# Kernel optimization log

Measured on AMD Instinct MI355X. Metric: run time of the kernel, lower is better.

## Reference

```python
import math
import jax, jax.numpy as jnp
import numpy as np

B, T, IDIM, D, H, L, DFF, CHUNK, LEFT = 8, 1024, 80, 512, 8, 6, 2048, 16, 4
DK = D // H
EPS = 1e-12  # espnet LayerNorm eps


def setup_inputs() -> dict:
    key = jax.random.key(0)
    it = iter(jax.random.split(key, 40))
    def nrm(shape, s=0.02):
        return jax.random.normal(next(it), shape, jnp.float32) * s
    return {
        "xs": jax.random.normal(next(it), (B, T, IDIM), jnp.float32),
        "masks": jnp.ones((B, 1, T), jnp.bool_),
        "emb_w": nrm((IDIM, D)), "emb_b": jnp.zeros((D,), jnp.float32),
        "emb_g": jnp.ones((D,), jnp.float32), "emb_beta": jnp.zeros((D,), jnp.float32),
        "wq": nrm((L, D, D)), "bq": jnp.zeros((L, D), jnp.float32),
        "wk": nrm((L, D, D)), "bk": jnp.zeros((L, D), jnp.float32),
        "wv": nrm((L, D, D)), "bv": jnp.zeros((L, D), jnp.float32),
        "wo": nrm((L, D, D)), "bo": jnp.zeros((L, D), jnp.float32),
        "ln1_g": jnp.ones((L, D), jnp.float32), "ln1_b": jnp.zeros((L, D), jnp.float32),
        "ln2_g": jnp.ones((L, D), jnp.float32), "ln2_b": jnp.zeros((L, D), jnp.float32),
        "ff1_w": nrm((L, D, DFF)), "ff1_b": jnp.zeros((L, DFF), jnp.float32),
        "ff2_w": nrm((L, DFF, D)), "ff2_b": jnp.zeros((L, D), jnp.float32),
        "fin_g": jnp.ones((D,), jnp.float32), "fin_b": jnp.zeros((D,), jnp.float32),
    }


def _ln(x, g, b):
    m = jnp.mean(x, -1, keepdims=True)
    v = jnp.mean((x - m) ** 2, -1, keepdims=True)
    return (x - m) / jnp.sqrt(v + EPS) * g + b


def _posenc(x):
    t, d = x.shape[1], x.shape[2]
    pos = jnp.arange(t, dtype=jnp.float32)[:, None]
    div = jnp.exp(jnp.arange(0, d, 2, dtype=jnp.float32) * (-math.log(10000.0) / d))
    pe = jnp.zeros((t, d), x.dtype)
    pe = pe.at[:, 0::2].set(jnp.sin(pos * div)).at[:, 1::2].set(jnp.cos(pos * div))
    return x * math.sqrt(d) + pe


def _mha(x, mask, wq, bq, wk, bk, wv, bv, wo, bo):
    b, t, _ = x.shape
    def split(w, bias):
        return (x @ w + bias).reshape(b, t, H, DK).transpose(0, 2, 1, 3)
    q, k, v = split(wq, bq), split(wk, bk), split(wv, bv)
    scores = jnp.einsum('bhqd,bhkd->bhqk', q, k) / math.sqrt(DK)
    m = mask[:, None]  # (B,1,1,T) for padding mask, (B,1,T,T) for chunk mask
    scores = jnp.where(m, scores, jnp.finfo(scores.dtype).min)
    attn = jnp.where(m, jax.nn.softmax(scores, axis=-1), 0.0)
    out = jnp.einsum('bhqk,bhkd->bhqd', attn, v).transpose(0, 2, 1, 3).reshape(b, t, D)
    return out @ wo + bo


def _stack(x, mask, p):
    # pre-norm (normalize_before=True, concat_after=False), dropout=0 (eval)
    for i in range(L):
        r = x
        h = _ln(x, p['ln1_g'][i], p['ln1_b'][i])
        x = r + _mha(h, mask, p['wq'][i], p['bq'][i], p['wk'][i], p['bk'][i],
                     p['wv'][i], p['bv'][i], p['wo'][i], p['bo'][i])
        r = x
        h = _ln(x, p['ln2_g'][i], p['ln2_b'][i])
        x = r + (jax.nn.relu(h @ p['ff1_w'][i] + p['ff1_b'][i]) @ p['ff2_w'][i] + p['ff2_b'][i])
    return x


def _chunk_mask(t):
    # equivalent to tril block mask with per-chunk triu window, kron'd with ones(chunk,chunk)
    nb = t // CHUNK
    i = jnp.arange(nb)
    blk = (i[None, :] <= i[:, None]) & (i[:, None] - i[None, :] <= LEFT)
    return jnp.repeat(jnp.repeat(blk, CHUNK, axis=0), CHUNK, axis=1)  # (t, t)


def reference(xs, masks, emb_w, emb_b, emb_g, emb_beta, wq, bq, wk, bk, wv, bv, wo, bo,
              ln1_g, ln1_b, ln2_g, ln2_b, ff1_w, ff1_b, ff2_w, ff2_b, fin_g, fin_b):
    p = dict(wq=wq, bq=bq, wk=wk, bk=bk, wv=wv, bv=bv, wo=wo, bo=bo,
             ln1_g=ln1_g, ln1_b=ln1_b, ln2_g=ln2_g, ln2_b=ln2_b,
             ff1_w=ff1_w, ff1_b=ff1_b, ff2_w=ff2_w, ff2_b=ff2_b)
    # embed: Linear -> LayerNorm -> Dropout(0) -> ReLU -> PositionalEncoding
    x = _posenc(jax.nn.relu(_ln(xs @ emb_w + emb_b, emb_g, emb_beta)))
    # offline pass: full padding mask
    xs_off = _ln(_stack(x, masks, p), fin_g, fin_b)
    # online pass: block-causal sliding-chunk mask & padding mask
    masks_on = _chunk_mask(x.shape[1])[None] & masks  # (B, T, T)
    xs_on = _ln(_stack(x, masks_on, p), fin_g, fin_b)
    return xs_off, xs_on, masks
```

## Files before the change

### kernel.cpp

```cpp
#include <hip/hip_runtime.h>
#include <hip/hip_bf16.h>
#include <cstdint>

typedef __hip_bfloat16 bf16;
typedef __attribute__((ext_vector_type(8))) short v8s;
typedef __attribute__((ext_vector_type(4))) float v4f;

#define SWZ(base, row, bytecol) ((base) + (row) * 128 + ((bytecol) ^ (((row) & 7) << 4)))

__device__ __forceinline__ void gload16(const void* g, void* l) {
  __builtin_amdgcn_global_load_lds((__attribute__((address_space(1))) void*)g,
                                   (__attribute__((address_space(3))) void*)l, 16, 0, 0);
}

__device__ __forceinline__ v4f mfma16(v8s a, v8s b, v4f c) {
  return __builtin_amdgcn_mfma_f32_16x16x32_bf16(a, b, c, 0, 0, 0);
}

__device__ __forceinline__ void pipe_barrier() {
  asm volatile("s_waitcnt lgkmcnt(0)" ::: "memory");
  __builtin_amdgcn_s_barrier();
  asm volatile("" ::: "memory");
}

__device__ __forceinline__ float bu2f(unsigned short u) {
  return __uint_as_float((unsigned)u << 16);
}
__device__ __forceinline__ unsigned short f2bu(float f) {
  bf16 b = __float2bfloat16(f);
  return *(unsigned short*)&b;
}
__device__ __forceinline__ unsigned packbf(float a, float b) {
  return (unsigned)f2bu(a) | ((unsigned)f2bu(b) << 16);
}

__device__ __forceinline__ float blocksum(float v, float* red, int tid) {
#pragma unroll
  for (int o = 32; o > 0; o >>= 1) v += __shfl_xor(v, o);
  if ((tid & 63) == 0) red[tid >> 6] = v;
  __syncthreads();
  float r = red[0] + red[1] + red[2] + red[3];
  __syncthreads();
  return r;
}

__global__ __launch_bounds__(256) void xsconv_kernel(const float* __restrict__ xs,
                                                     bf16* __restrict__ dst) {
  const int i = blockIdx.x * 256 + threadIdx.x;
  if (i >= 8192 * 128) return;
  const int row = i >> 7, col = i & 127;
  dst[i] = __float2bfloat16(col < 80 ? xs[row * 80 + col] : 0.0f);
}

__global__ __launch_bounds__(256) void embwconv_kernel(const float* __restrict__ w,
                                                       bf16* __restrict__ dst) {
  const int i = blockIdx.x * 256 + threadIdx.x;
  if (i >= 512 * 128) return;
  const int n = i >> 7, k = i & 127;
  dst[i] = __float2bfloat16(k < 80 ? w[k * 512 + n] : 0.0f);
}

__global__ __launch_bounds__(256) void posenc_ln_kernel(
    const bf16* __restrict__ e, const float* __restrict__ g, const float* __restrict__ beta,
    const float* __restrict__ ln1g, const float* __restrict__ ln1b, bf16* __restrict__ x,
    bf16* __restrict__ h, int zdim) {
  const int tok = blockIdx.x;
  const int tid = threadIdx.x;
  __shared__ float red[4];
  const int c0 = 2 * tid, c1 = 2 * tid + 1;
  const unsigned ev = *(const unsigned*)(e + (long)tok * 512 + c0);
  float v0 = bu2f((unsigned short)ev);
  float v1 = bu2f((unsigned short)(ev >> 16));
  const float mean = blocksum(v0 + v1, red, tid) * (1.0f / 512.0f);
  const float d0 = v0 - mean, d1 = v1 - mean;
  const float var = blocksum(d0 * d0 + d1 * d1, red, tid) * (1.0f / 512.0f);
  const float inv = rsqrtf(var + 1e-12f);
  const float r0 = fmaxf(d0 * inv * g[c0] + beta[c0], 0.0f);
  const float r1 = fmaxf(d1 * inv * g[c1] + beta[c1], 0.0f);
  const int t = tok & 1023;
  const float a = (float)t * __expf((float)c0 * (-9.210340371976184f / 512.0f));
  float sa, ca;
  __sincosf(a, &sa, &ca);
  const float x0 = r0 * 22.627416997969522f + sa;
  const float x1 = r1 * 22.627416997969522f + ca;
  const float m2 = blocksum(x0 + x1, red, tid) * (1.0f / 512.0f);
  const float e0 = x0 - m2, e1 = x1 - m2;
  const float vv = blocksum(e0 * e0 + e1 * e1, red, tid) * (1.0f / 512.0f);
  const float iv = rsqrtf(vv + 1e-12f);
  const float h0 = e0 * iv * ln1g[c0] + ln1b[c0];
  const float h1 = e1 * iv * ln1g[c1] + ln1b[c1];
  const unsigned xp = packbf(x0, x1);
  const unsigned hp = packbf(h0, h1);
  for (int z = 0; z < zdim; ++z) {
    const long row = tok + (long)z * 8192;
    *(unsigned*)(x + row * 512 + c0) = xp;
    *(unsigned*)(h + row * 512 + c0) = hp;
  }
}

template <int FINAL>
__global__ __launch_bounds__(256) void add_ln_kernel(bf16* __restrict__ x,
                                                     const bf16* __restrict__ y,
                                                     const float* __restrict__ g,
                                                     const float* __restrict__ bta,
                                                     void* __restrict__ outp) {
  const long row = blockIdx.x;
  const int tid = threadIdx.x;
  __shared__ float red[4];
  const int c0 = 2 * tid;
  const long i0 = row * 512 + c0;
  const unsigned xv = *(const unsigned*)(x + i0);
  const unsigned yv = *(const unsigned*)(y + i0);
  const float v0 = bu2f((unsigned short)xv) + bu2f((unsigned short)yv);
  const float v1 = bu2f((unsigned short)(xv >> 16)) + bu2f((unsigned short)(yv >> 16));
  if (!FINAL)
    *(unsigned*)(x + i0) = packbf(v0, v1);
  const float mean = blocksum(v0 + v1, red, tid) * (1.0f / 512.0f);
  const float d0 = v0 - mean, d1 = v1 - mean;
  const float var = blocksum(d0 * d0 + d1 * d1, red, tid) * (1.0f / 512.0f);
  const float inv = rsqrtf(var + 1e-12f);
  const float y0 = d0 * inv * g[c0] + bta[c0];
  const float y1 = d1 * inv * g[c0 + 1] + bta[c0 + 1];
  if (FINAL) {
    float2* o = (float2*)outp;
    o[i0 >> 1] = make_float2(y0, y1);
  } else {
    *(unsigned*)((bf16*)outp + i0) = packbf(y0, y1);
  }
}

__global__ __launch_bounds__(256) void trconv_kernel(const float* __restrict__ src,
                                                     bf16* __restrict__ dst, int K, int N,
                                                     long src_lstride, long dst_lstride) {
  __shared__ float tile[32][33];
  src += (long)blockIdx.z * src_lstride;
  dst += (long)blockIdx.z * dst_lstride;
  const int n0 = blockIdx.x * 32, k0 = blockIdx.y * 32;
  const int tx = threadIdx.x & 31, ty = threadIdx.x >> 5;
#pragma unroll
  for (int i = 0; i < 32; i += 8)
    tile[ty + i][tx] = src[(long)(k0 + ty + i) * N + n0 + tx];
  __syncthreads();
#pragma unroll
  for (int i = 0; i < 32; i += 8)
    dst[(long)(n0 + ty + i) * K + k0 + tx] = __float2bfloat16(tile[tx][ty + i]);
}

__global__ void biascat_kernel(const float* bq, const float* bk, const float* bv, float* o) {
  const int i = blockIdx.x * 256 + threadIdx.x;
  if (i >= 6 * 1536) return;
  const int l = i / 1536, n = i % 1536;
  o[i] = (n < 512) ? bq[l * 512 + n] : (n < 1024) ? bk[l * 512 + n - 512] : bv[l * 512 + n - 1024];
}

__global__ void maskout_kernel(const int* m, float* o, int n) {
  const int i = blockIdx.x * 256 + threadIdx.x;
  if (i < n) o[i] = m[i] ? 1.0f : 0.0f;
}

template <bool RELU>
__global__ __launch_bounds__(256) void gemm_kernel(const bf16* __restrict__ A,
                                                   const bf16* __restrict__ W,
                                                   const float* __restrict__ bias,
                                                   bf16* __restrict__ outp, int M, int N, int K) {
  __shared__ __align__(16) bf16 As[2][128 * 64];
  __shared__ __align__(16) bf16 Bs[2][128 * 64];
  const int tid = threadIdx.x, lane = tid & 63, wave = tid >> 6;
  int bx, by;
  {
    const int gx = gridDim.x, gy = gridDim.y;
    const int f = (int)blockIdx.y * gx + (int)blockIdx.x;
    if ((gx & 7) == 0) {
      const int xcd = f & 7;
      const int j = f >> 3;
      const int per = gx >> 3;
      by = j % gy;
      bx = xcd * per + j / gy;
    } else {
      bx = blockIdx.x;
      by = blockIdx.y;
    }
  }
  const int m0 = bx * 128, n0 = by * 128;
  const int wr = (wave >> 1) * 64, wc = (wave & 1) * 64;
  const int colswz = (((tid & 7) ^ ((tid >> 3) & 7)) * 8);
  const bf16* ag = A + (long)(m0 + (tid >> 3)) * K + colswz;
  const bf16* bg = W + (long)(n0 + (tid >> 3)) * K + colswz;
  char* asb = (char*)As + wave * 1024;
  char* bsb = (char*)Bs + wave * 1024;
  v4f acc[4][4] = {};
  const int frow = lane & 15, fch = lane >> 4;
  const int nk = K >> 6;
#pragma unroll
  for (int i = 0; i < 4; ++i) {
    gload16(ag + (long)i * 32 * K, asb + i * 4096);
    gload16(bg + (long)i * 32 * K, bsb + i * 4096);
  }
  for (int t = 0; t < nk; ++t) {
    const int cur = t & 1;
    asm volatile("s_waitcnt vmcnt(0)" ::: "memory");
    __builtin_amdgcn_s_barrier();
    if (t + 1 < nk) {
      const int k0 = (t + 1) << 6;
      const int nb = (cur ^ 1) * 16384;
#pragma unroll
      for (int i = 0; i < 4; ++i) {
        gload16(ag + k0 + (long)i * 32 * K, asb + nb + i * 4096);
        gload16(bg + k0 + (long)i * 32 * K, bsb + nb + i * 4096);
      }
    }
    const char* Ab = (const char*)As[cur];
    const char* Bb = (const char*)Bs[cur];
#pragma unroll
    for (int kk = 0; kk < 2; ++kk) {
      v8s af[4], bfv[4];
#pragma unroll
      for (int m = 0; m < 4; ++m) {
        const int row = wr + m * 16 + frow;
        af[m] = *(const v8s*)(Ab + row * 128 + (((kk * 4 + fch) * 16) ^ ((row & 7) << 4)));
      }
#pragma unroll
      for (int n = 0; n < 4; ++n) {
        const int row = wc + n * 16 + frow;
        bfv[n] = *(const v8s*)(Bb + row * 128 + (((kk * 4 + fch) * 16) ^ ((row & 7) << 4)));
      }
#pragma unroll
      for (int m = 0; m < 4; ++m)
#pragma unroll
        for (int n = 0; n < 4; ++n)
          acc[m][n] = mfma16(af[m], bfv[n], acc[m][n]);
    }
  }
  float bv[4];
#pragma unroll
  for (int n = 0; n < 4; ++n) bv[n] = bias[n0 + wc + n * 16 + frow];
#pragma unroll
  for (int m = 0; m < 4; ++m) {
#pragma unroll
    for (int n = 0; n < 4; ++n) {
#pragma unroll
      for (int r = 0; r < 4; ++r) {
        const int row = m0 + wr + m * 16 + fch * 4 + r;
        const int col = n0 + wc + n * 16 + frow;
        float v = acc[m][n][r] + bv[n];
        if (RELU) v = fmaxf(v, 0.0f);
        outp[(long)row * N + col] = __float2bfloat16(v);
      }
    }
  }
}

__global__ __launch_bounds__(512) void attn_kernel(const bf16* __restrict__ qkv,
                                                   bf16* __restrict__ aout, int chunk0) {
  __shared__ __align__(16) char QPs[128 * 128];
  __shared__ __align__(16) char Ks[2][64 * 128];
  __shared__ __align__(16) char Vs[2][64 * 128];
  const int tid = threadIdx.x, lane = tid & 63, wave = tid >> 6;
  int qb, bh, zz;
  {
    const int zdim = (int)gridDim.z;
    const int nwg = 512 * zdim;
    const int flat = (int)blockIdx.x + 8 * (int)blockIdx.y + 512 * (int)blockIdx.z;
    const int s = (flat & 7) * (nwg >> 3) + (flat >> 3);
    qb = s & 7;
    const int rest = s >> 3;
    zz = rest & (zdim - 1);
    bh = rest >> (zdim >> 1);
  }
  const int chunked = chunk0 + zz;
  const long tb = (long)zz * 8192 + (long)(bh >> 3) * 1024;
  const int hh = bh & 7;
  const int q0 = qb * 128;
  const int sr = tid >> 3, ss = tid & 7;
  int kt0 = 0, kt1 = 16;
  if (chunked) {
    kt0 = qb * 2 - 1;
    if (kt0 < 0) kt0 = 0;
    kt1 = qb * 2 + 2;
  }
  uint4 kreg, vreg;
  {
    const long ro = (tb + kt0 * 64 + sr) * 1536 + hh * 64 + ss * 8;
    kreg = *(const uint4*)(qkv + ro + 512);
    vreg = *(const uint4*)(qkv + ro + 1024);
  }
#pragma unroll
  for (int p = 0; p < 2; ++p) {
    const int rr = sr + p * 64;
    const uint4 d = *(const uint4*)(qkv + (tb + q0 + rr) * 1536 + hh * 64 + ss * 8);
    *(uint4*)(QPs + rr * 128 + ((ss * 16) ^ ((rr & 7) << 4))) = d;
  }
  pipe_barrier();
  const int frow = lane & 15, fch = lane >> 4;
  const v8s qa0 = *(const v8s*)SWZ(QPs, wave * 16 + frow, fch * 16);
  const v8s qa1 = *(const v8s*)SWZ(QPs, wave * 16 + frow, 64 + fch * 16);
  *(uint4*)(Ks[0] + sr * 128 + ((ss * 16) ^ ((sr & 7) << 4))) = kreg;
  {
    const bf16* ve = (const bf16*)&vreg;
#pragma unroll
    for (int e = 0; e < 8; ++e) {
      *(bf16*)(Vs[0] + (ss * 8 + e) * 128 + ((sr * 2) ^ (ss << 4) ^ (e << 4))) = ve[e];
    }
  }
  if (kt0 + 1 < kt1) {
    const long ro = (tb + (kt0 + 1) * 64 + sr) * 1536 + hh * 64 + ss * 8;
    kreg = *(const uint4*)(qkv + ro + 512);
    vreg = *(const uint4*)(qkv + ro + 1024);
  }
  pipe_barrier();
  v4f accv[4] = {};
  float m_run = -1e30f, l_run = 0.0f;
  const int qswz = (frow & 7) << 4;
  char* Pw = QPs + wave * 2048;
  const int qb_ = (q0 + wave * 16 + frow) >> 4;
  int cur = 0;
  for (int kt = kt0; kt < kt1; ++kt) {
    if (kt + 1 < kt1) {
      *(uint4*)(Ks[cur ^ 1] + sr * 128 + ((ss * 16) ^ ((sr & 7) << 4))) = kreg;
      const bf16* ve = (const bf16*)&vreg;
#pragma unroll
      for (int e = 0; e < 8; ++e) {
        *(bf16*)(Vs[cur ^ 1] + (ss * 8 + e) * 128 + ((sr * 2) ^ (ss << 4) ^ (e << 4))) = ve[e];
      }
      if (kt + 2 < kt1) {
        const long ro = (tb + (kt + 2) * 64 + sr) * 1536 + hh * 64 + ss * 8;
        kreg = *(const uint4*)(qkv + ro + 512);
        vreg = *(const uint4*)(qkv + ro + 1024);
      }
    }
    const char* Kc = Ks[cur];
    const char* Vc = Vs[cur];
    v4f s4[4];
    __builtin_amdgcn_s_setprio(1);
#pragma unroll
    for (int n = 0; n < 4; ++n) {
      const v8s kb0 = *(const v8s*)SWZ(Kc, n * 16 + frow, fch * 16);
      const v8s kb1 = *(const v8s*)SWZ(Kc, n * 16 + frow, 64 + fch * 16);
      v4f z = {0.f, 0.f, 0.f, 0.f};
      z = mfma16(kb0, qa0, z);
      z = mfma16(kb1, qa1, z);
      s4[n] = z * 0.125f;
    }
    __builtin_amdgcn_s_setprio(0);
    if (chunked) {
#pragma unroll
      for (int n = 0; n < 4; ++n)
#pragma unroll
        for (int r = 0; r < 4; ++r) {
          const int kb_ = (kt * 64 + n * 16 + fch * 4 + r) >> 4;
          if (!(kb_ <= qb_ && qb_ - kb_ <= 4)) s4[n][r] = -1e30f;
        }
    }
    float u0 = fmaxf(fmaxf(s4[0][0], s4[1][0]), fmaxf(s4[2][0], s4[3][0]));
    float u1 = fmaxf(fmaxf(s4[0][1], s4[1][1]), fmaxf(s4[2][1], s4[3][1]));
    float u2 = fmaxf(fmaxf(s4[0][2], s4[1][2]), fmaxf(s4[2][2], s4[3][2]));
    float u3 = fmaxf(fmaxf(s4[0][3], s4[1][3]), fmaxf(s4[2][3], s4[3][3]));
    float mt = fmaxf(fmaxf(u0, u1), fmaxf(u2, u3));
    mt = fmaxf(mt, __shfl_xor(mt, 16));
    mt = fmaxf(mt, __shfl_xor(mt, 32));
    const float mnew = fmaxf(m_run, mt);
    const float esc = __expf(m_run - mnew);
#pragma unroll
    for (int n = 0; n < 4; ++n)
#pragma unroll
      for (int r = 0; r < 4; ++r) s4[n][r] = __expf(s4[n][r] - mnew);
    float t0 = (s4[0][0] + s4[1][0]) + (s4[2][0] + s4[3][0]);
    float t1 = (s4[0][1] + s4[1][1]) + (s4[2][1] + s4[3][1]);
    float t2 = (s4[0][2] + s4[1][2]) + (s4[2][2] + s4[3][2]);
    float t3 = (s4[0][3] + s4[1][3]) + (s4[2][3] + s4[3][3]);
    float st = (t0 + t1) + (t2 + t3);
    st += __shfl_xor(st, 16);
    st += __shfl_xor(st, 32);
    l_run = l_run * esc + st;
    m_run = mnew;
#pragma unroll
    for (int f = 0; f < 4; ++f)
#pragma unroll
      for (int r = 0; r < 4; ++r) accv[f][r] *= esc;
#pragma unroll
    for (int n = 0; n < 4; ++n) {
      uint2 w;
      w.x = packbf(s4[n][0], s4[n][1]);
      w.y = packbf(s4[n][2], s4[n][3]);
      *(uint2*)(Pw + frow * 128 + ((fch * 8 + 32 * n) ^ qswz)) = w;
    }
    const v8s pa0 = *(const v8s*)(Pw + frow * 128 + ((fch * 16) ^ qswz));
    const v8s pa1 = *(const v8s*)(Pw + frow * 128 + ((64 + fch * 16) ^ qswz));
    __builtin_amdgcn_s_setprio(1);
#pragma unroll
    for (int f = 0; f < 4; ++f) {
      const int vh = (((f * 2 + (frow >> 3)) ^ (frow & 7)) & 7) << 4;
      const int drow = (f * 16 + frow) * 128;
      const v8s vb0 = *(const v8s*)(Vc + drow + ((fch * 16) ^ vh));
      const v8s vb1 = *(const v8s*)(Vc + drow + ((64 + fch * 16) ^ vh));
      accv[f] = mfma16(vb0, pa0, accv[f]);
      accv[f] = mfma16(vb1, pa1, accv[f]);
    }
    __builtin_amdgcn_s_setprio(0);
    pipe_barrier();
    cur ^= 1;
  }
  const float rl = 1.0f / l_run;
  const long orow = (tb + q0 + wave * 16 + frow) * 512 + hh * 64;
#pragma unroll
  for (int f = 0; f < 4; ++f) {
    uint2 u;
    u.x = packbf(accv[f][0] * rl, accv[f][1] * rl);
    u.y = packbf(accv[f][2] * rl, accv[f][3] * rl);
    *(uint2*)(aout + orow + f * 16 + fch * 4) = u;
  }
}

struct Bufs {
  bf16 *Wqkv, *Wo, *W1, *W2;
  float* bqkv;
  bf16 *xsbf, *wemb, *e;
  bf16* x;
  bf16 *h, *qkv, *attn;
  size_t need;
};

static Bufs make_layout(char* ws, long rows) {
  size_t off = 0;
  auto al = [&](size_t b) -> void* {
    void* p = ws + off;
    off += (b + 255) & ~(size_t)255;
    return p;
  };
  Bufs B;
  B.Wqkv = (bf16*)al((size_t)6 * 1536 * 512 * 2);
  B.Wo = (bf16*)al((size_t)6 * 512 * 512 * 2);
  B.W1 = (bf16*)al((size_t)6 * 2048 * 512 * 2);
  B.W2 = (bf16*)al((size_t)6 * 512 * 2048 * 2);
  B.bqkv = (float*)al((size_t)6 * 1536 * 4);
  B.xsbf = (bf16*)al((size_t)8192 * 128 * 2);
  B.wemb = (bf16*)al((size_t)512 * 128 * 2);
  B.e = (bf16*)al((size_t)8192 * 512 * 2);
  B.x = (bf16*)al((size_t)rows * 512 * 2);
  B.h = (bf16*)al((size_t)rows * 512 * 2);
  B.qkv = (bf16*)al((size_t)rows * 1536 * 2);
  B.attn = (bf16*)al((size_t)rows * 512 * 2);
  B.need = off;
  return B;
}

extern "C" void kernel_launch(void* const* d_in, const int* in_sizes, int n_in, void* d_out,
                              int out_size, void* d_ws, size_t ws_size, hipStream_t stream) {
  const float* xs = (const float*)d_in[0];
  const int* masks = (const int*)d_in[1];
  const float* emb_w = (const float*)d_in[2];
  const float* emb_b = (const float*)d_in[3];
  const float* emb_g = (const float*)d_in[4];
  const float* emb_beta = (const float*)d_in[5];
  const float* wq = (const float*)d_in[6];
  const float* bq = (const float*)d_in[7];
  const float* wk = (const float*)d_in[8];
  const float* bk = (const float*)d_in[9];
  const float* wv = (const float*)d_in[10];
  const float* bv = (const float*)d_in[11];
  const float* wo = (const float*)d_in[12];
  const float* bo = (const float*)d_in[13];
  const float* ln1g = (const float*)d_in[14];
  const float* ln1b = (const float*)d_in[15];
  const float* ln2g = (const float*)d_in[16];
  const float* ln2b = (const float*)d_in[17];
  const float* f1w = (const float*)d_in[18];
  const float* f1b = (const float*)d_in[19];
  const float* f2w = (const float*)d_in[20];
  const float* f2b = (const float*)d_in[21];
  const float* fing = (const float*)d_in[22];
  const float* finb = (const float*)d_in[23];

  char* ws = (char*)d_ws;
  Bufs bm = make_layout(ws, 16384);
  const bool merged = bm.need <= ws_size;
  Bufs b = merged ? bm : make_layout(ws, 8192);
  const long rows = merged ? 16384 : 8192;
  const int npass = merged ? 1 : 2;
  const int mg = (int)(rows / 128);
  const int zdim = (int)(rows / 8192);

  trconv_kernel<<<dim3(16, 16, 6), 256, 0, stream>>>(wq, b.Wqkv, 512, 512, (long)512 * 512,
                                                     (long)1536 * 512);
  trconv_kernel<<<dim3(16, 16, 6), 256, 0, stream>>>(wk, b.Wqkv + 512 * 512, 512, 512,
                                                     (long)512 * 512, (long)1536 * 512);
  trconv_kernel<<<dim3(16, 16, 6), 256, 0, stream>>>(wv, b.Wqkv + 1024 * 512, 512, 512,
                                                     (long)512 * 512, (long)1536 * 512);
  trconv_kernel<<<dim3(16, 16, 6), 256, 0, stream>>>(wo, b.Wo, 512, 512, (long)512 * 512,
                                                     (long)512 * 512);
  trconv_kernel<<<dim3(64, 16, 6), 256, 0, stream>>>(f1w, b.W1, 512, 2048, (long)512 * 2048,
                                                     (long)2048 * 512);
  trconv_kernel<<<dim3(16, 64, 6), 256, 0, stream>>>(f2w, b.W2, 2048, 512, (long)2048 * 512,
                                                     (long)512 * 2048);
  biascat_kernel<<<36, 256, 0, stream>>>(bq, bk, bv, b.bqkv);
  xsconv_kernel<<<(8192 * 128 + 255) / 256, 256, 0, stream>>>(xs, b.xsbf);
  embwconv_kernel<<<(512 * 128 + 255) / 256, 256, 0, stream>>>(emb_w, b.wemb);

  for (int pass = 0; pass < npass; ++pass) {
    gemm_kernel<false><<<dim3(64, 4), 256, 0, stream>>>(b.xsbf, b.wemb, emb_b, b.e, 8192, 512,
                                                        128);
    posenc_ln_kernel<<<8192, 256, 0, stream>>>(b.e, emb_g, emb_beta, ln1g, ln1b, b.x, b.h, zdim);
    for (int l = 0; l < 6; ++l) {
      gemm_kernel<false><<<dim3(mg, 12), 256, 0, stream>>>(
          b.h, b.Wqkv + (size_t)l * 1536 * 512, b.bqkv + l * 1536, b.qkv, (int)rows, 1536, 512);
      attn_kernel<<<dim3(8, 64, zdim), 512, 0, stream>>>(b.qkv, b.attn, merged ? 0 : pass);
      gemm_kernel<false><<<dim3(mg, 4), 256, 0, stream>>>(
          b.attn, b.Wo + (size_t)l * 512 * 512, bo + l * 512, b.h, (int)rows, 512, 512);
      add_ln_kernel<0><<<(int)rows, 256, 0, stream>>>(b.x, b.h, ln2g + l * 512, ln2b + l * 512,
                                                      b.h);
      gemm_kernel<true><<<dim3(mg, 16), 256, 0, stream>>>(
          b.h, b.W1 + (size_t)l * 2048 * 512, f1b + l * 2048, b.qkv , (int)rows, 2048, 512);
      gemm_kernel<false><<<dim3(mg, 4), 256, 0, stream>>>(
          b.qkv , b.W2 + (size_t)l * 512 * 2048, f2b + l * 512, b.h, (int)rows, 512, 2048);
      if (l < 5)
        add_ln_kernel<0><<<(int)rows, 256, 0, stream>>>(b.x, b.h, ln1g + (l + 1) * 512,
                                                        ln1b + (l + 1) * 512, b.h);
      else
        add_ln_kernel<1><<<(int)rows, 256, 0, stream>>>(
            b.x, b.h, fing, finb, (float*)d_out + (size_t)pass * 8192 * 512);
    }
  }
  maskout_kernel<<<32, 256, 0, stream>>>(masks, (float*)d_out + (size_t)2 * 8192 * 512, 8192);
  (void)in_sizes;
  (void)n_in;
  (void)out_size;
}
```

Before: 1.385 ms.

## Fuse residual add into GEMM epilogue, vectorize stores, lazy softmax rescale

The Wo and FF2 GEMMs now add their output straight into the residual stream x in the epilogue. The separate add+LayerNorm kernels become pure LayerNorm kernels, which removes one bf16 read and write of the hidden state per sublayer. The GEMM swaps MFMA operand order so each lane holds four consecutive columns, which allows vectorized bias loads and 8-byte stores. Attention now uses exp2 with a folded scale, skips the running-max rescale when the max barely grows, and defers the row-sum shuffle reduction to the end. These changes trade some numerical headroom and extra read-modify-write traffic in the epilogue for fewer kernel passes.

```diff
diff --git a/kernel.cpp b/kernel.cpp
--- a/kernel.cpp
+++ b/kernel.cpp
@@ -99,22 +99,18 @@
 }
 
 template <int FINAL>
-__global__ __launch_bounds__(256) void add_ln_kernel(bf16* __restrict__ x,
-                                                     const bf16* __restrict__ y,
-                                                     const float* __restrict__ g,
-                                                     const float* __restrict__ bta,
-                                                     void* __restrict__ outp) {
+__global__ __launch_bounds__(256) void ln2_kernel(const bf16* __restrict__ x,
+                                                  const float* __restrict__ g,
+                                                  const float* __restrict__ bta,
+                                                  void* __restrict__ outp) {
   const long row = blockIdx.x;
   const int tid = threadIdx.x;
   __shared__ float red[4];
   const int c0 = 2 * tid;
   const long i0 = row * 512 + c0;
   const unsigned xv = *(const unsigned*)(x + i0);
-  const unsigned yv = *(const unsigned*)(y + i0);
-  const float v0 = bu2f((unsigned short)xv) + bu2f((unsigned short)yv);
-  const float v1 = bu2f((unsigned short)(xv >> 16)) + bu2f((unsigned short)(yv >> 16));
-  if (!FINAL)
-    *(unsigned*)(x + i0) = packbf(v0, v1);
+  const float v0 = bu2f((unsigned short)xv);
+  const float v1 = bu2f((unsigned short)(xv >> 16));
   const float mean = blocksum(v0 + v1, red, tid) * (1.0f / 512.0f);
   const float d0 = v0 - mean, d1 = v1 - mean;
   const float var = blocksum(d0 * d0 + d1 * d1, red, tid) * (1.0f / 512.0f);
@@ -158,7 +154,7 @@
   if (i < n) o[i] = m[i] ? 1.0f : 0.0f;
 }
 
-template <bool RELU>
+template <int MODE, bool RELU>
 __global__ __launch_bounds__(256) void gemm_kernel(const bf16* __restrict__ A,
                                                    const bf16* __restrict__ W,
                                                    const float* __restrict__ bias,
@@ -228,24 +224,36 @@
       for (int m = 0; m < 4; ++m)
 #pragma unroll
         for (int n = 0; n < 4; ++n)
-          acc[m][n] = mfma16(af[m], bfv[n], acc[m][n]);
-    }
-  }
-  float bv[4];
-#pragma unroll
-  for (int n = 0; n < 4; ++n) bv[n] = bias[n0 + wc + n * 16 + frow];
-#pragma unroll
-  for (int m = 0; m < 4; ++m) {
-#pragma unroll
-    for (int n = 0; n < 4; ++n) {
-#pragma unroll
-      for (int r = 0; r < 4; ++r) {
-        const int row = m0 + wr + m * 16 + fch * 4 + r;
-        const int col = n0 + wc + n * 16 + frow;
-        float v = acc[m][n][r] + bv[n];
-        if (RELU) v = fmaxf(v, 0.0f);
-        outp[(long)row * N + col] = __float2bfloat16(v);
-      }
+          acc[m][n] = mfma16(bfv[n], af[m], acc[m][n]);
+    }
+  }
+  const int colb = n0 + wc + fch * 4;
+#pragma unroll
+  for (int n = 0; n < 4; ++n) {
+    const float4 bv4 = *(const float4*)(bias + colb + n * 16);
+#pragma unroll
+    for (int m = 0; m < 4; ++m) {
+      const long row = m0 + wr + m * 16 + frow;
+      bf16* op = outp + row * N + colb + n * 16;
+      float a0 = acc[m][n][0] + bv4.x, a1 = acc[m][n][1] + bv4.y;
+      float a2 = acc[m][n][2] + bv4.z, a3 = acc[m][n][3] + bv4.w;
+      if (RELU) {
+        a0 = fmaxf(a0, 0.0f);
+        a1 = fmaxf(a1, 0.0f);
+        a2 = fmaxf(a2, 0.0f);
+        a3 = fmaxf(a3, 0.0f);
+      }
+      if (MODE == 1) {
+        const uint2 xv = *(const uint2*)op;
+        a0 += bu2f((unsigned short)xv.x);
+        a1 += bu2f((unsigned short)(xv.x >> 16));
+        a2 += bu2f((unsigned short)xv.y);
+        a3 += bu2f((unsigned short)(xv.y >> 16));
+      }
+      uint2 u;
+      u.x = packbf(a0, a1);
+      u.y = packbf(a2, a3);
+      *(uint2*)op = u;
     }
   }
 }
@@ -310,6 +318,7 @@
   pipe_barrier();
   v4f accv[4] = {};
   float m_run = -1e30f, l_run = 0.0f;
+  const float C = 0.18033688011112042f;
   const int qswz = (frow & 7) << 4;
   char* Pw = QPs + wave * 2048;
   const int qb_ = (q0 + wave * 16 + frow) >> 4;
@@ -339,7 +348,7 @@
       v4f z = {0.f, 0.f, 0.f, 0.f};
       z = mfma16(kb0, qa0, z);
       z = mfma16(kb1, qa1, z);
-      s4[n] = z * 0.125f;
+      s4[n] = z;
     }
     __builtin_amdgcn_s_setprio(0);
     if (chunked) {
@@ -358,25 +367,24 @@
     float mt = fmaxf(fmaxf(u0, u1), fmaxf(u2, u3));
     mt = fmaxf(mt, __shfl_xor(mt, 16));
     mt = fmaxf(mt, __shfl_xor(mt, 32));
-    const float mnew = fmaxf(m_run, mt);
-    const float esc = __expf(m_run - mnew);
+    if (!__all(mt <= m_run + 63.77f)) {
+      const float mnew = fmaxf(m_run, mt);
+      const float esc = exp2f((m_run - mnew) * C);
+      l_run *= esc;
+#pragma unroll
+      for (int f = 0; f < 4; ++f)
+#pragma unroll
+        for (int r = 0; r < 4; ++r) accv[f][r] *= esc;
+      m_run = mnew;
+    }
 #pragma unroll
     for (int n = 0; n < 4; ++n)
 #pragma unroll
-      for (int r = 0; r < 4; ++r) s4[n][r] = __expf(s4[n][r] - mnew);
-    float t0 = (s4[0][0] + s4[1][0]) + (s4[2][0] + s4[3][0]);
-    float t1 = (s4[0][1] + s4[1][1]) + (s4[2][1] + s4[3][1]);
-    float t2 = (s4[0][2] + s4[1][2]) + (s4[2][2] + s4[3][2]);
-    float t3 = (s4[0][3] + s4[1][3]) + (s4[2][3] + s4[3][3]);
-    float st = (t0 + t1) + (t2 + t3);
-    st += __shfl_xor(st, 16);
-    st += __shfl_xor(st, 32);
-    l_run = l_run * esc + st;
-    m_run = mnew;
-#pragma unroll
-    for (int f = 0; f < 4; ++f)
-#pragma unroll
-      for (int r = 0; r < 4; ++r) accv[f][r] *= esc;
+      for (int r = 0; r < 4; ++r) s4[n][r] = exp2f((s4[n][r] - m_run) * C);
+    l_run += ((s4[0][0] + s4[1][0]) + (s4[2][0] + s4[3][0])) +
+             ((s4[0][1] + s4[1][1]) + (s4[2][1] + s4[3][1])) +
+             ((s4[0][2] + s4[1][2]) + (s4[2][2] + s4[3][2])) +
+             ((s4[0][3] + s4[1][3]) + (s4[2][3] + s4[3][3]));
 #pragma unroll
     for (int n = 0; n < 4; ++n) {
       uint2 w;
@@ -400,6 +408,8 @@
     pipe_barrier();
     cur ^= 1;
   }
+  l_run += __shfl_xor(l_run, 16);
+  l_run += __shfl_xor(l_run, 32);
   const float rl = 1.0f / l_run;
   const long orow = (tb + q0 + wave * 16 + frow) * 512 + hh * 64;
 #pragma unroll
@@ -497,27 +507,26 @@
   embwconv_kernel<<<(512 * 128 + 255) / 256, 256, 0, stream>>>(emb_w, b.wemb);
 
   for (int pass = 0; pass < npass; ++pass) {
-    gemm_kernel<false><<<dim3(64, 4), 256, 0, stream>>>(b.xsbf, b.wemb, emb_b, b.e, 8192, 512,
-                                                        128);
+    gemm_kernel<0, false><<<dim3(64, 4), 256, 0, stream>>>(b.xsbf, b.wemb, emb_b, b.e, 8192, 512,
+                                                           128);
     posenc_ln_kernel<<<8192, 256, 0, stream>>>(b.e, emb_g, emb_beta, ln1g, ln1b, b.x, b.h, zdim);
     for (int l = 0; l < 6; ++l) {
-      gemm_kernel<false><<<dim3(mg, 12), 256, 0, stream>>>(
+      gemm_kernel<0, false><<<dim3(mg, 12), 256, 0, stream>>>(
           b.h, b.Wqkv + (size_t)l * 1536 * 512, b.bqkv + l * 1536, b.qkv, (int)rows, 1536, 512);
       attn_kernel<<<dim3(8, 64, zdim), 512, 0, stream>>>(b.qkv, b.attn, merged ? 0 : pass);
-      gemm_kernel<false><<<dim3(mg, 4), 256, 0, stream>>>(
-          b.attn, b.Wo + (size_t)l * 512 * 512, bo + l * 512, b.h, (int)rows, 512, 512);
-      add_ln_kernel<0><<<(int)rows, 256, 0, stream>>>(b.x, b.h, ln2g + l * 512, ln2b + l * 512,
-                                                      b.h);
-      gemm_kernel<true><<<dim3(mg, 16), 256, 0, stream>>>(
+      gemm_kernel<1, false><<<dim3(mg, 4), 256, 0, stream>>>(
+          b.attn, b.Wo + (size_t)l * 512 * 512, bo + l * 512, b.x, (int)rows, 512, 512);
+      ln2_kernel<0><<<(int)rows, 256, 0, stream>>>(b.x, ln2g + l * 512, ln2b + l * 512, b.h);
+      gemm_kernel<0, true><<<dim3(mg, 16), 256, 0, stream>>>(
           b.h, b.W1 + (size_t)l * 2048 * 512, f1b + l * 2048, b.qkv , (int)rows, 2048, 512);
-      gemm_kernel<false><<<dim3(mg, 4), 256, 0, stream>>>(
-          b.qkv , b.W2 + (size_t)l * 512 * 2048, f2b + l * 512, b.h, (int)rows, 512, 2048);
+      gemm_kernel<1, false><<<dim3(mg, 4), 256, 0, stream>>>(
+          b.qkv , b.W2 + (size_t)l * 512 * 2048, f2b + l * 512, b.x, (int)rows, 512, 2048);
       if (l < 5)
-        add_ln_kernel<0><<<(int)rows, 256, 0, stream>>>(b.x, b.h, ln1g + (l + 1) * 512,
-                                                        ln1b + (l + 1) * 512, b.h);
+        ln2_kernel<0><<<(int)rows, 256, 0, stream>>>(b.x, ln1g + (l + 1) * 512,
+                                                     ln1b + (l + 1) * 512, b.h);
       else
-        add_ln_kernel<1><<<(int)rows, 256, 0, stream>>>(
-            b.x, b.h, fing, finb, (float*)d_out + (size_t)pass * 8192 * 512);
+        ln2_kernel<1><<<(int)rows, 256, 0, stream>>>(b.x, fing, finb,
+                                                     (float*)d_out + (size_t)pass * 8192 * 512);
     }
   }
   maskout_kernel<<<32, 256, 0, stream>>>(masks, (float*)d_out + (size_t)2 * 8192 * 512, 8192);
```

Measured after the change: 1.557 ms. +12.4%, slower.
